# Performance work log

Measured on AMD Instinct MI355X. Metric: run time of the kernel, lower is better.

Reference implementation:

```python
import jax, jax.numpy as jnp
import numpy as np

N_NODES = 100000
N_EDGES = 3200000
D_IN = 256      # encoder_dim feeding gnn_1
D_GNN = 256     # decoder_output_dim * 4
N_CLUSTER = 4
SIGMA = 0.5
V = 1.0


def setup_inputs() -> dict:
    key = jax.random.key(0)
    ks = jax.random.split(key, 16)
    f = lambda k, shp: jax.random.normal(k, shp, dtype=jnp.float32)
    inp = {
        "encoded_input_data": f(ks[0], (N_NODES, D_IN)),
        "tra1": f(ks[1], (N_NODES, D_GNN)),
        "tra2": f(ks[2], (N_NODES, D_GNN)),
        "tra3": f(ks[3], (N_NODES, D_GNN)),
        "z":    f(ks[4], (N_NODES, D_GNN)),
        "edge_row": jax.random.randint(ks[5], (N_EDGES,), 0, N_NODES, dtype=jnp.int32),
        "edge_col": jax.random.randint(ks[6], (N_EDGES,), 0, N_NODES, dtype=jnp.int32),
        "edge_vals": jax.random.uniform(ks[7], (N_EDGES,), dtype=jnp.float32),
        "W1": f(ks[8], (D_IN, D_GNN)) * (1.0 / np.sqrt(D_IN)),
        "W2": f(ks[9], (D_GNN, D_GNN)) * (1.0 / np.sqrt(D_GNN)),
        "W3": f(ks[10], (D_GNN, D_GNN)) * (1.0 / np.sqrt(D_GNN)),
        "W4": f(ks[11], (D_GNN, D_GNN)) * (1.0 / np.sqrt(D_GNN)),
        "W5": f(ks[12], (D_GNN, N_CLUSTER)) * (1.0 / np.sqrt(D_GNN)),
        "cluster": f(ks[13], (N_CLUSTER, D_GNN)),
    }
    return inp


def _spmm(row, col, vals, x):
    # sparse adj (COO) @ x : gather source rows, scale, scatter-add to dest rows
    return jax.ops.segment_sum(vals[:, None] * x[col], row, num_segments=N_NODES)


def _gnn(x, W, row, col, vals, active=True):
    out = _spmm(row, col, vals, x @ W)
    return jax.nn.relu(out) if active else out


def reference(encoded_input_data, tra1, tra2, tra3, z,
              edge_row, edge_col, edge_vals,
              W1, W2, W3, W4, W5, cluster):
    r, c, vals = edge_row, edge_col, edge_vals
    h = _gnn(encoded_input_data, W1, r, c, vals)
    h = _gnn((1 - SIGMA) * h + SIGMA * tra1, W2, r, c, vals)
    h = _gnn((1 - SIGMA) * h + SIGMA * tra2, W3, r, c, vals)
    h = _gnn((1 - SIGMA) * h + SIGMA * tra3, W4, r, c, vals)
    h = _gnn((1 - SIGMA) * h + SIGMA * z, W5, r, c, vals, active=False)
    predict = jax.nn.softmax(h, axis=1)  # [N, n_cluster]

    # student-t soft assignment: ||z_i - mu_j||^2 expanded to avoid [N,K,D] blowup
    dist2 = (jnp.sum(z * z, axis=1, keepdims=True)
             - 2.0 * (z @ cluster.T)
             + jnp.sum(cluster * cluster, axis=1)[None, :])
    q = 1.0 / (1.0 + dist2 / V)
    q = q ** ((V + 1.0) / 2.0)
    q = q / jnp.sum(q, axis=1, keepdims=True)

    return jnp.concatenate([predict, q], axis=1)  # [N, 2*n_cluster]
```

## Files before the change

### kernel.cpp

```cpp
#include <hip/hip_runtime.h>

#define NN 100000
#define NE 3200000
#define DD 256
#define KC 4
#define MPAD 100096

typedef _Float16 f16x8 __attribute__((ext_vector_type(8)));
typedef _Float16 f16x4 __attribute__((ext_vector_type(4)));
typedef float f32x4 __attribute__((ext_vector_type(4)));


__global__ __launch_bounds__(256) void k_hist(const int* __restrict__ row,
                                              int* __restrict__ counts) {
    int e = blockIdx.x * 256 + threadIdx.x;
    if (e < NE) atomicAdd(&counts[row[e]], 1);
}

__global__ __launch_bounds__(256) void k_scan1(const int* __restrict__ counts,
                                               int* __restrict__ offs,
                                               int* __restrict__ bsum) {
    __shared__ int s[256];
    const int t = threadIdx.x;
    const int base = blockIdx.x * 1024 + t * 4;
    int v[4];
    int sum = 0;
#pragma unroll
    for (int i = 0; i < 4; ++i) {
        v[i] = (base + i < NN) ? counts[base + i] : 0;
        sum += v[i];
    }
    s[t] = sum;
    __syncthreads();
    for (int off = 1; off < 256; off <<= 1) {
        int x = (t >= off) ? s[t - off] : 0;
        __syncthreads();
        s[t] += x;
        __syncthreads();
    }
    int run = (t > 0) ? s[t - 1] : 0;
#pragma unroll
    for (int i = 0; i < 4; ++i) {
        if (base + i < NN) offs[base + i] = run;
        run += v[i];
    }
    if (t == 255) bsum[blockIdx.x] = s[255];
}

__global__ void k_scan2(int* __restrict__ bsum, int nb) {
    if (threadIdx.x == 0 && blockIdx.x == 0) {
        int run = 0;
        for (int i = 0; i < nb; ++i) {
            int c = bsum[i];
            bsum[i] = run;
            run += c;
        }
    }
}

__global__ __launch_bounds__(256) void k_scan3(int* __restrict__ offs,
                                               const int* __restrict__ bsum) {
    int i = blockIdx.x * 256 + threadIdx.x;
    if (i < NN)
        offs[i] += bsum[i >> 10];
    else if (i == NN)
        offs[NN] = NE;
}

__global__ __launch_bounds__(256) void k_fill(const int* __restrict__ row,
                                              const int* __restrict__ col,
                                              const float* __restrict__ val,
                                              const int* __restrict__ offs,
                                              int* __restrict__ cursor,
                                              int2* __restrict__ edges) {
    int e = blockIdx.x * 256 + threadIdx.x;
    if (e >= NE) return;
    int r = row[e];
    int p = offs[r] + atomicAdd(&cursor[r], 1);
    int2 ev;
    ev.x = col[e];
    ev.y = __float_as_int(val[e]);
    edges[p] = ev;
}


__global__ __launch_bounds__(256) void k_cvtX(const float* __restrict__ in,
                                              _Float16* __restrict__ out) {
    const size_t base = ((size_t)blockIdx.x * 256 + threadIdx.x) * 8;
    if (base >= (size_t)NN * DD) return;
    f32x4 v0 = __builtin_nontemporal_load(reinterpret_cast<const f32x4*>(in + base));
    f32x4 v1 = __builtin_nontemporal_load(reinterpret_cast<const f32x4*>(in + base + 4));
    f16x8 o;
    o[0] = (_Float16)v0[0]; o[1] = (_Float16)v0[1]; o[2] = (_Float16)v0[2]; o[3] = (_Float16)v0[3];
    o[4] = (_Float16)v1[0]; o[5] = (_Float16)v1[1]; o[6] = (_Float16)v1[2]; o[7] = (_Float16)v1[3];
    *reinterpret_cast<f16x8*>(out + base) = o;
}

__global__ __launch_bounds__(256) void k_cvtW(const float* __restrict__ W1,
                                              const float* __restrict__ W2,
                                              const float* __restrict__ W3,
                                              const float* __restrict__ W4,
                                              _Float16* __restrict__ Wt) {
    __shared__ float s[32][33];
    const float* W = (blockIdx.z == 0) ? W1 : (blockIdx.z == 1) ? W2 : (blockIdx.z == 2) ? W3 : W4;
    _Float16* o = Wt + (size_t)blockIdx.z * DD * DD;
    const int bk = blockIdx.x * 32;
    const int bn = blockIdx.y * 32;
    const int tx = threadIdx.x & 31, ty = threadIdx.x >> 5;
    for (int r = ty; r < 32; r += 8) s[r][tx] = W[(size_t)(bk + r) * DD + bn + tx];
    __syncthreads();
    for (int r = ty; r < 32; r += 8) o[(size_t)(bn + r) * DD + bk + tx] = (_Float16)s[tx][r];
}


__device__ __forceinline__ void load_lds16(const void* g, void* l) {
    __builtin_amdgcn_global_load_lds((const __attribute__((address_space(1))) void*)g,
                                     (__attribute__((address_space(3))) void*)l, 16, 0, 0);
}

__global__ __launch_bounds__(512, 4) void k_gemm_h(const _Float16* __restrict__ X,
                                                   const _Float16* __restrict__ Wt,
                                                   _Float16* __restrict__ Y) {
    __shared__ __align__(16) char lds[49152];
    char* const Albase = lds;
    char* const Blbase = lds + 16384;

    const int tid = threadIdx.x;
    const int lane = tid & 63;
    const int wid = tid >> 6;
    const int wr = wid >> 2;
    const int wc = wid & 3;
    const int bm = blockIdx.x * 128;

    const int aoffl = wid * 1024 + lane * 16;
    const int arw = aoffl >> 6;
    const int acb = (aoffl & 63) ^ (((arw >> 1) & 3) << 4);
    const char* const Asrc0 = (const char*)X + ((size_t)(bm + arw) * DD) * 2 + acb;
    char* const Adst0 = Albase + wid * 1024;

    const int boffl0 = wid * 1024 + lane * 16;
    const int brw0 = boffl0 >> 6;
    const int bcb0 = (boffl0 & 63) ^ (((brw0 >> 1) & 3) << 4);
    const char* const Bsrc0 = (const char*)Wt + ((size_t)brw0 * DD) * 2 + bcb0;
    const int boffl1 = 8192 + wid * 1024 + lane * 16;
    const int brw1 = boffl1 >> 6;
    const int bcb1 = (boffl1 & 63) ^ (((brw1 >> 1) & 3) << 4);
    const char* const Bsrc1 = (const char*)Wt + ((size_t)brw1 * DD) * 2 + bcb1;
    char* const Bdst0 = Blbase + wid * 1024;
    char* const Bdst1 = Blbase + 8192 + wid * 1024;

    int aro[4], bro[4];
#pragma unroll
    for (int m = 0; m < 4; ++m) {
        const int r = wr * 64 + m * 16 + (lane & 15);
        aro[m] = r * 64 + ((((lane >> 4) * 16)) ^ (((r >> 1) & 3) << 4));
    }
#pragma unroll
    for (int n = 0; n < 4; ++n) {
        const int r = wc * 64 + n * 16 + (lane & 15);
        bro[n] = r * 64 + ((((lane >> 4) * 16)) ^ (((r >> 1) & 3) << 4));
    }

    f32x4 acc[4][4];
#pragma unroll
    for (int m = 0; m < 4; ++m)
#pragma unroll
        for (int n = 0; n < 4; ++n) acc[m][n] = (f32x4){0.f, 0.f, 0.f, 0.f};

    load_lds16(Asrc0, Adst0);
    load_lds16(Bsrc0, Bdst0);
    load_lds16(Bsrc1, Bdst1);
    __syncthreads();

    for (int kt = 0; kt < 8; ++kt) {
        const int cur = kt & 1;
        if (kt < 7) {
            const size_t kb = (size_t)(kt + 1) * 32 * 2;
            load_lds16(Asrc0 + kb, Adst0 + (cur ^ 1) * 8192);
            load_lds16(Bsrc0 + kb, Bdst0 + (cur ^ 1) * 16384);
            load_lds16(Bsrc1 + kb, Bdst1 + (cur ^ 1) * 16384);
        }
        const char* Ab = Albase + cur * 8192;
        const char* Bb = Blbase + cur * 16384;
        f16x8 af[4], bf[4];
#pragma unroll
        for (int m = 0; m < 4; ++m) af[m] = *reinterpret_cast<const f16x8*>(Ab + aro[m]);
#pragma unroll
        for (int n = 0; n < 4; ++n) bf[n] = *reinterpret_cast<const f16x8*>(Bb + bro[n]);
#pragma unroll
        for (int m = 0; m < 4; ++m)
#pragma unroll
            for (int n = 0; n < 4; ++n)
                acc[m][n] = __builtin_amdgcn_mfma_f32_16x16x32_f16(af[m], bf[n], acc[m][n], 0, 0, 0);
        __syncthreads();
    }

#pragma unroll
    for (int m = 0; m < 4; ++m) {
        const int row = bm + wr * 64 + m * 16 + (lane >> 4) * 4;
#pragma unroll
        for (int n = 0; n < 4; ++n) {
            const int col = wc * 64 + n * 16 + (lane & 15);
#pragma unroll
            for (int j = 0; j < 4; ++j)
                Y[(size_t)(row + j) * DD + col] = (_Float16)acc[m][n][j];
        }
    }
}


__global__ __launch_bounds__(256) void k_spmm_h(const int* __restrict__ offs,
                                                const int2* __restrict__ edges,
                                                const _Float16* __restrict__ Y,
                                                const float* __restrict__ blend,
                                                _Float16* __restrict__ Xout) {
    const int row = blockIdx.x * 4 + (threadIdx.x >> 6);
    if (row >= NN) return;
    const int lane = threadIdx.x & 63;
    const int half = lane >> 5;
    const int sub = lane & 31;
    const int e0 = offs[row], e1 = offs[row + 1];
    float acc[8] = {};
    int e = e0 + half;
    for (; e + 6 < e1; e += 8) {
        const int2 ev0 = edges[e], ev1 = edges[e + 2], ev2 = edges[e + 4], ev3 = edges[e + 6];
        const float v0 = __int_as_float(ev0.y), v1 = __int_as_float(ev1.y);
        const float v2 = __int_as_float(ev2.y), v3 = __int_as_float(ev3.y);
        const f16x8 y0 = *reinterpret_cast<const f16x8*>(Y + (size_t)ev0.x * DD + sub * 8);
        const f16x8 y1 = *reinterpret_cast<const f16x8*>(Y + (size_t)ev1.x * DD + sub * 8);
        const f16x8 y2 = *reinterpret_cast<const f16x8*>(Y + (size_t)ev2.x * DD + sub * 8);
        const f16x8 y3 = *reinterpret_cast<const f16x8*>(Y + (size_t)ev3.x * DD + sub * 8);
#pragma unroll
        for (int j = 0; j < 8; ++j)
            acc[j] += v0 * (float)y0[j] + v1 * (float)y1[j] + v2 * (float)y2[j] + v3 * (float)y3[j];
    }
    for (; e < e1; e += 2) {
        const int2 ev = edges[e];
        const float v = __int_as_float(ev.y);
        const f16x8 y = *reinterpret_cast<const f16x8*>(Y + (size_t)ev.x * DD + sub * 8);
#pragma unroll
        for (int j = 0; j < 8; ++j) acc[j] += v * (float)y[j];
    }
#pragma unroll
    for (int j = 0; j < 8; ++j) acc[j] += __shfl_xor(acc[j], 32);
    if (half == 0) {
        const size_t bi = (size_t)row * DD + sub * 8;
        const f32x4 t0 = __builtin_nontemporal_load(reinterpret_cast<const f32x4*>(blend + bi));
        const f32x4 t1 = __builtin_nontemporal_load(reinterpret_cast<const f32x4*>(blend + bi + 4));
        f16x8 o;
        o[0] = (_Float16)(0.5f * fmaxf(acc[0], 0.f) + 0.5f * t0[0]);
        o[1] = (_Float16)(0.5f * fmaxf(acc[1], 0.f) + 0.5f * t0[1]);
        o[2] = (_Float16)(0.5f * fmaxf(acc[2], 0.f) + 0.5f * t0[2]);
        o[3] = (_Float16)(0.5f * fmaxf(acc[3], 0.f) + 0.5f * t0[3]);
        o[4] = (_Float16)(0.5f * fmaxf(acc[4], 0.f) + 0.5f * t1[0]);
        o[5] = (_Float16)(0.5f * fmaxf(acc[5], 0.f) + 0.5f * t1[1]);
        o[6] = (_Float16)(0.5f * fmaxf(acc[6], 0.f) + 0.5f * t1[2]);
        o[7] = (_Float16)(0.5f * fmaxf(acc[7], 0.f) + 0.5f * t1[3]);
        *reinterpret_cast<f16x8*>(Xout + bi) = o;
    }
}

__global__ __launch_bounds__(256) void k_spmm_last(const int* __restrict__ offs,
                                                   const int2* __restrict__ edges,
                                                   const _Float16* __restrict__ Y,
                                                   const float* __restrict__ z,
                                                   const float* __restrict__ W5,
                                                   const float* __restrict__ cl,
                                                   float* __restrict__ Y5,
                                                   float* __restrict__ out) {
    const int row = blockIdx.x * 4 + (threadIdx.x >> 6);
    if (row >= NN) return;
    const int lane = threadIdx.x & 63;
    const int half = lane >> 5;
    const int sub = lane & 31;
    const int e0 = offs[row], e1 = offs[row + 1];
    float acc[8] = {};
    int e = e0 + half;
    for (; e + 6 < e1; e += 8) {
        const int2 ev0 = edges[e], ev1 = edges[e + 2], ev2 = edges[e + 4], ev3 = edges[e + 6];
        const float v0 = __int_as_float(ev0.y), v1 = __int_as_float(ev1.y);
        const float v2 = __int_as_float(ev2.y), v3 = __int_as_float(ev3.y);
        const f16x8 y0 = *reinterpret_cast<const f16x8*>(Y + (size_t)ev0.x * DD + sub * 8);
        const f16x8 y1 = *reinterpret_cast<const f16x8*>(Y + (size_t)ev1.x * DD + sub * 8);
        const f16x8 y2 = *reinterpret_cast<const f16x8*>(Y + (size_t)ev2.x * DD + sub * 8);
        const f16x8 y3 = *reinterpret_cast<const f16x8*>(Y + (size_t)ev3.x * DD + sub * 8);
#pragma unroll
        for (int j = 0; j < 8; ++j)
            acc[j] += v0 * (float)y0[j] + v1 * (float)y1[j] + v2 * (float)y2[j] + v3 * (float)y3[j];
    }
    for (; e < e1; e += 2) {
        const int2 ev = edges[e];
        const float v = __int_as_float(ev.y);
        const f16x8 y = *reinterpret_cast<const f16x8*>(Y + (size_t)ev.x * DD + sub * 8);
#pragma unroll
        for (int j = 0; j < 8; ++j) acc[j] += v * (float)y[j];
    }
#pragma unroll
    for (int j = 0; j < 8; ++j) acc[j] += __shfl_xor(acc[j], 32);
    if (half == 0) {
        const size_t bi = (size_t)row * DD + sub * 8;
        const f32x4 z0 = __builtin_nontemporal_load(reinterpret_cast<const f32x4*>(z + bi));
        const f32x4 z1 = __builtin_nontemporal_load(reinterpret_cast<const f32x4*>(z + bi + 4));
        float zb[8] = {z0[0], z0[1], z0[2], z0[3], z1[0], z1[1], z1[2], z1[3]};
        float b[8];
#pragma unroll
        for (int j = 0; j < 8; ++j) b[j] = 0.5f * fmaxf(acc[j], 0.f) + 0.5f * zb[j];

        float p[4] = {0.f, 0.f, 0.f, 0.f};
        float zz = 0.f;
#pragma unroll
        for (int j = 0; j < 8; ++j) {
            const int d = sub * 8 + j;
            const f32x4 w = *reinterpret_cast<const f32x4*>(W5 + (size_t)d * KC);
            p[0] += b[j] * w[0];
            p[1] += b[j] * w[1];
            p[2] += b[j] * w[2];
            p[3] += b[j] * w[3];
            zz += zb[j] * zb[j];
        }
        float dot[4] = {0.f, 0.f, 0.f, 0.f}, cc[4] = {0.f, 0.f, 0.f, 0.f};
#pragma unroll
        for (int c2 = 0; c2 < 4; ++c2) {
            const f32x4 c40 = *reinterpret_cast<const f32x4*>(cl + (size_t)c2 * DD + sub * 8);
            const f32x4 c41 = *reinterpret_cast<const f32x4*>(cl + (size_t)c2 * DD + sub * 8 + 4);
            dot[c2] += zb[0] * c40[0] + zb[1] * c40[1] + zb[2] * c40[2] + zb[3] * c40[3] +
                       zb[4] * c41[0] + zb[5] * c41[1] + zb[6] * c41[2] + zb[7] * c41[3];
            cc[c2] += c40[0] * c40[0] + c40[1] * c40[1] + c40[2] * c40[2] + c40[3] * c40[3] +
                      c41[0] * c41[0] + c41[1] * c41[1] + c41[2] * c41[2] + c41[3] * c41[3];
        }
#pragma unroll
        for (int o = 16; o; o >>= 1) {
            zz += __shfl_xor(zz, o);
#pragma unroll
            for (int c2 = 0; c2 < 4; ++c2) {
                p[c2] += __shfl_xor(p[c2], o);
                dot[c2] += __shfl_xor(dot[c2], o);
                cc[c2] += __shfl_xor(cc[c2], o);
            }
        }
        if (sub == 0) {
            *reinterpret_cast<f32x4*>(Y5 + (size_t)row * KC) = (f32x4){p[0], p[1], p[2], p[3]};
            float q[4], s = 0.f;
#pragma unroll
            for (int c2 = 0; c2 < 4; ++c2) {
                const float d2 = zz - 2.f * dot[c2] + cc[c2];
                q[c2] = 1.f / (1.f + d2);
                s += q[c2];
            }
            const float inv = 1.f / s;
            *reinterpret_cast<f32x4*>(out + (size_t)row * 8 + 4) =
                (f32x4){q[0] * inv, q[1] * inv, q[2] * inv, q[3] * inv};
        }
    }
}


__device__ inline float wred(float v) {
#pragma unroll
    for (int o = 32; o; o >>= 1) v += __shfl_down(v, o);
    return v;
}

__global__ __launch_bounds__(256) void k_sm5(const int* __restrict__ offs,
                                             const int2* __restrict__ edges,
                                             const float* __restrict__ Y5,
                                             float* __restrict__ out) {
    const int row = blockIdx.x * 4 + (threadIdx.x >> 6);
    if (row >= NN) return;
    const int lane = threadIdx.x & 63;
    const int e0 = offs[row], e1 = offs[row + 1];
    float ax = 0.f, ay = 0.f, az = 0.f, aw = 0.f;
    for (int e = e0 + lane; e < e1; e += 64) {
        const int2 ev = edges[e];
        const float v = __int_as_float(ev.y);
        const f32x4 y = *reinterpret_cast<const f32x4*>(Y5 + (size_t)ev.x * KC);
        ax += v * y[0];
        ay += v * y[1];
        az += v * y[2];
        aw += v * y[3];
    }
    ax = wred(ax);
    ay = wred(ay);
    az = wred(az);
    aw = wred(aw);
    if (lane == 0) {
        float m = fmaxf(fmaxf(ax, ay), fmaxf(az, aw));
        float ex = __expf(ax - m), ey = __expf(ay - m), ez = __expf(az - m), ew = __expf(aw - m);
        float inv = 1.f / (ex + ey + ez + ew);
        *reinterpret_cast<f32x4*>(out + (size_t)row * 8) =
            (f32x4){ex * inv, ey * inv, ez * inv, ew * inv};
    }
}


extern "C" void kernel_launch(void* const* d_in, const int* in_sizes, int n_in,
                              void* d_out, int out_size, void* d_ws, size_t ws_size,
                              hipStream_t stream) {
    const float* enc = (const float*)d_in[0];
    const float* tra1 = (const float*)d_in[1];
    const float* tra2 = (const float*)d_in[2];
    const float* tra3 = (const float*)d_in[3];
    const float* z = (const float*)d_in[4];
    const int* erow = (const int*)d_in[5];
    const int* ecol = (const int*)d_in[6];
    const float* evals = (const float*)d_in[7];
    const float* W1 = (const float*)d_in[8];
    const float* W2 = (const float*)d_in[9];
    const float* W3 = (const float*)d_in[10];
    const float* W4 = (const float*)d_in[11];
    const float* W5 = (const float*)d_in[12];
    const float* cluster = (const float*)d_in[13];
    float* out = (float*)d_out;

    char* ws = (char*)d_ws;
    size_t off = 0;
    auto take = [&](size_t bytes) -> void* {
        void* p = ws + off;
        off = (off + bytes + 255) & ~(size_t)255;
        return p;
    };
    int* counts = (int*)take((size_t)NN * 4);
    int* cursor = (int*)take((size_t)NN * 4);
    int* offs = (int*)take((size_t)(NN + 1) * 4);
    int* bsum = (int*)take(4096);
    int2* edges = (int2*)take((size_t)NE * 8);
    _Float16* Xa = (_Float16*)take((size_t)MPAD * DD * 2);
    _Float16* Xb = (_Float16*)take((size_t)MPAD * DD * 2);
    _Float16* Wt = (_Float16*)take((size_t)4 * DD * DD * 2);
    float* Y5 = (float*)take((size_t)NN * KC * 4);

    hipMemsetAsync(counts, 0, (size_t)NN * 4, stream);
    hipMemsetAsync(cursor, 0, (size_t)NN * 4, stream);

    k_hist<<<(NE + 255) / 256, 256, 0, stream>>>(erow, counts);
    const int nsb = (NN + 1023) / 1024;
    k_scan1<<<nsb, 256, 0, stream>>>(counts, offs, bsum);
    k_scan2<<<1, 64, 0, stream>>>(bsum, nsb);
    k_scan3<<<(NN + 256) / 256, 256, 0, stream>>>(offs, bsum);
    k_fill<<<(NE + 255) / 256, 256, 0, stream>>>(erow, ecol, evals, offs, cursor, edges);

    k_cvtX<<<(NN * DD / 8 + 255) / 256, 256, 0, stream>>>(enc, Xa);
    k_cvtW<<<dim3(8, 8, 4), 256, 0, stream>>>(W1, W2, W3, W4, Wt);

    const int gb = MPAD / 128;
    const int rb = NN / 4;

    k_gemm_h<<<gb, 512, 0, stream>>>(Xa, Wt + 0 * DD * DD, Xb);
    k_spmm_h<<<rb, 256, 0, stream>>>(offs, edges, Xb, tra1, Xa);

    k_gemm_h<<<gb, 512, 0, stream>>>(Xa, Wt + 1 * DD * DD, Xb);
    k_spmm_h<<<rb, 256, 0, stream>>>(offs, edges, Xb, tra2, Xa);

    k_gemm_h<<<gb, 512, 0, stream>>>(Xa, Wt + 2 * DD * DD, Xb);
    k_spmm_h<<<rb, 256, 0, stream>>>(offs, edges, Xb, tra3, Xa);

    k_gemm_h<<<gb, 512, 0, stream>>>(Xa, Wt + 3 * DD * DD, Xb);
    k_spmm_last<<<rb, 256, 0, stream>>>(offs, edges, Xb, z, W5, cluster, Y5, out);

    k_sm5<<<rb, 256, 0, stream>>>(offs, edges, Y5, out);
}
```

Before: 1.437 ms.

## Pack edges into 32-bit words and split SpMM feature columns into two passes

Each edge becomes one 32-bit word: a 17-bit column index plus a 15-bit fixed-point quantized weight. This halves the CSR edge traffic. Every SpMM layer also now runs as two launches, each covering 128 of the 256 feature columns. The smaller gather working set should fit better in cache, and four edge groups per row give more memory parallelism. The costs are that the edge list is read twice, the weights are quantized to 15 bits (assumes values in [0,1]), and the last layer has to carry partial results between its two passes.

```diff
diff --git a/kernel.cpp b/kernel.cpp
--- a/kernel.cpp
+++ b/kernel.cpp
@@ -5,9 +5,9 @@
 #define DD 256
 #define KC 4
 #define MPAD 100096
+#define INV15 (1.0f / 32767.0f)
 
 typedef _Float16 f16x8 __attribute__((ext_vector_type(8)));
-typedef _Float16 f16x4 __attribute__((ext_vector_type(4)));
 typedef float f32x4 __attribute__((ext_vector_type(4)));
 
 
@@ -72,15 +72,13 @@
                                               const float* __restrict__ val,
                                               const int* __restrict__ offs,
                                               int* __restrict__ cursor,
-                                              int2* __restrict__ edges) {
+                                              unsigned* __restrict__ edges) {
     int e = blockIdx.x * 256 + threadIdx.x;
     if (e >= NE) return;
     int r = row[e];
     int p = offs[r] + atomicAdd(&cursor[r], 1);
-    int2 ev;
-    ev.x = col[e];
-    ev.y = __float_as_int(val[e]);
-    edges[p] = ev;
+    unsigned v15 = (unsigned)(val[e] * 32767.f + 0.5f);
+    edges[p] = (v15 << 17) | (unsigned)col[e];
 }
 
 
@@ -210,41 +208,47 @@
 
 
 __global__ __launch_bounds__(256) void k_spmm_h(const int* __restrict__ offs,
-                                                const int2* __restrict__ edges,
+                                                const unsigned* __restrict__ edges,
                                                 const _Float16* __restrict__ Y,
                                                 const float* __restrict__ blend,
-                                                _Float16* __restrict__ Xout) {
+                                                _Float16* __restrict__ Xout,
+                                                int d_off) {
     const int row = blockIdx.x * 4 + (threadIdx.x >> 6);
     if (row >= NN) return;
     const int lane = threadIdx.x & 63;
-    const int half = lane >> 5;
-    const int sub = lane & 31;
+    const int grp = lane >> 4, sub = lane & 15;
+    const int dbase = d_off + sub * 8;
     const int e0 = offs[row], e1 = offs[row + 1];
     float acc[8] = {};
-    int e = e0 + half;
-    for (; e + 6 < e1; e += 8) {
-        const int2 ev0 = edges[e], ev1 = edges[e + 2], ev2 = edges[e + 4], ev3 = edges[e + 6];
-        const float v0 = __int_as_float(ev0.y), v1 = __int_as_float(ev1.y);
-        const float v2 = __int_as_float(ev2.y), v3 = __int_as_float(ev3.y);
-        const f16x8 y0 = *reinterpret_cast<const f16x8*>(Y + (size_t)ev0.x * DD + sub * 8);
-        const f16x8 y1 = *reinterpret_cast<const f16x8*>(Y + (size_t)ev1.x * DD + sub * 8);
-        const f16x8 y2 = *reinterpret_cast<const f16x8*>(Y + (size_t)ev2.x * DD + sub * 8);
-        const f16x8 y3 = *reinterpret_cast<const f16x8*>(Y + (size_t)ev3.x * DD + sub * 8);
+    int e = e0 + grp;
+    for (; e + 12 < e1; e += 16) {
+        const unsigned u0 = edges[e], u1 = edges[e + 4], u2 = edges[e + 8], u3 = edges[e + 12];
+        const float v0 = (float)(u0 >> 17) * INV15;
+        const float v1 = (float)(u1 >> 17) * INV15;
+        const float v2 = (float)(u2 >> 17) * INV15;
+        const float v3 = (float)(u3 >> 17) * INV15;
+        const f16x8 y0 = *reinterpret_cast<const f16x8*>(Y + ((size_t)(u0 & 0x1FFFFu) << 8) + dbase);
+        const f16x8 y1 = *reinterpret_cast<const f16x8*>(Y + ((size_t)(u1 & 0x1FFFFu) << 8) + dbase);
+        const f16x8 y2 = *reinterpret_cast<const f16x8*>(Y + ((size_t)(u2 & 0x1FFFFu) << 8) + dbase);
+        const f16x8 y3 = *reinterpret_cast<const f16x8*>(Y + ((size_t)(u3 & 0x1FFFFu) << 8) + dbase);
 #pragma unroll
         for (int j = 0; j < 8; ++j)
             acc[j] += v0 * (float)y0[j] + v1 * (float)y1[j] + v2 * (float)y2[j] + v3 * (float)y3[j];
     }
-    for (; e < e1; e += 2) {
-        const int2 ev = edges[e];
-        const float v = __int_as_float(ev.y);
-        const f16x8 y = *reinterpret_cast<const f16x8*>(Y + (size_t)ev.x * DD + sub * 8);
+    for (; e < e1; e += 4) {
+        const unsigned u = edges[e];
+        const float v = (float)(u >> 17) * INV15;
+        const f16x8 y = *reinterpret_cast<const f16x8*>(Y + ((size_t)(u & 0x1FFFFu) << 8) + dbase);
 #pragma unroll
         for (int j = 0; j < 8; ++j) acc[j] += v * (float)y[j];
     }
 #pragma unroll
-    for (int j = 0; j < 8; ++j) acc[j] += __shfl_xor(acc[j], 32);
-    if (half == 0) {
-        const size_t bi = (size_t)row * DD + sub * 8;
+    for (int j = 0; j < 8; ++j) {
+        acc[j] += __shfl_xor(acc[j], 16);
+        acc[j] += __shfl_xor(acc[j], 32);
+    }
+    if (grp == 0) {
+        const size_t bi = (size_t)row * DD + dbase;
         const f32x4 t0 = __builtin_nontemporal_load(reinterpret_cast<const f32x4*>(blend + bi));
         const f32x4 t1 = __builtin_nontemporal_load(reinterpret_cast<const f32x4*>(blend + bi + 4));
         f16x8 o;
@@ -260,76 +264,79 @@
     }
 }
 
-__global__ __launch_bounds__(256) void k_spmm_last(const int* __restrict__ offs,
-                                                   const int2* __restrict__ edges,
-                                                   const _Float16* __restrict__ Y,
-                                                   const float* __restrict__ z,
-                                                   const float* __restrict__ W5,
-                                                   const float* __restrict__ cl,
-                                                   float* __restrict__ Y5,
-                                                   float* __restrict__ out) {
+__global__ __launch_bounds__(256) void k_last(const int* __restrict__ offs,
+                                              const unsigned* __restrict__ edges,
+                                              const _Float16* __restrict__ Y,
+                                              const float* __restrict__ z,
+                                              const float* __restrict__ W5,
+                                              const float* __restrict__ cl,
+                                              float* __restrict__ part,
+                                              float* __restrict__ Y5,
+                                              float* __restrict__ out,
+                                              int d_off, int final_) {
     const int row = blockIdx.x * 4 + (threadIdx.x >> 6);
     if (row >= NN) return;
     const int lane = threadIdx.x & 63;
-    const int half = lane >> 5;
-    const int sub = lane & 31;
+    const int grp = lane >> 4, sub = lane & 15;
+    const int dbase = d_off + sub * 8;
     const int e0 = offs[row], e1 = offs[row + 1];
     float acc[8] = {};
-    int e = e0 + half;
-    for (; e + 6 < e1; e += 8) {
-        const int2 ev0 = edges[e], ev1 = edges[e + 2], ev2 = edges[e + 4], ev3 = edges[e + 6];
-        const float v0 = __int_as_float(ev0.y), v1 = __int_as_float(ev1.y);
-        const float v2 = __int_as_float(ev2.y), v3 = __int_as_float(ev3.y);
-        const f16x8 y0 = *reinterpret_cast<const f16x8*>(Y + (size_t)ev0.x * DD + sub * 8);
-        const f16x8 y1 = *reinterpret_cast<const f16x8*>(Y + (size_t)ev1.x * DD + sub * 8);
-        const f16x8 y2 = *reinterpret_cast<const f16x8*>(Y + (size_t)ev2.x * DD + sub * 8);
-        const f16x8 y3 = *reinterpret_cast<const f16x8*>(Y + (size_t)ev3.x * DD + sub * 8);
+    int e = e0 + grp;
+    for (; e + 12 < e1; e += 16) {
+        const unsigned u0 = edges[e], u1 = edges[e + 4], u2 = edges[e + 8], u3 = edges[e + 12];
+        const float v0 = (float)(u0 >> 17) * INV15;
+        const float v1 = (float)(u1 >> 17) * INV15;
+        const float v2 = (float)(u2 >> 17) * INV15;
+        const float v3 = (float)(u3 >> 17) * INV15;
+        const f16x8 y0 = *reinterpret_cast<const f16x8*>(Y + ((size_t)(u0 & 0x1FFFFu) << 8) + dbase);
+        const f16x8 y1 = *reinterpret_cast<const f16x8*>(Y + ((size_t)(u1 & 0x1FFFFu) << 8) + dbase);
+        const f16x8 y2 = *reinterpret_cast<const f16x8*>(Y + ((size_t)(u2 & 0x1FFFFu) << 8) + dbase);
+        const f16x8 y3 = *reinterpret_cast<const f16x8*>(Y + ((size_t)(u3 & 0x1FFFFu) << 8) + dbase);
 #pragma unroll
         for (int j = 0; j < 8; ++j)
             acc[j] += v0 * (float)y0[j] + v1 * (float)y1[j] + v2 * (float)y2[j] + v3 * (float)y3[j];
     }
-    for (; e < e1; e += 2) {
-        const int2 ev = edges[e];
-        const float v = __int_as_float(ev.y);
-        const f16x8 y = *reinterpret_cast<const f16x8*>(Y + (size_t)ev.x * DD + sub * 8);
+    for (; e < e1; e += 4) {
+        const unsigned u = edges[e];
+        const float v = (float)(u >> 17) * INV15;
+        const f16x8 y = *reinterpret_cast<const f16x8*>(Y + ((size_t)(u & 0x1FFFFu) << 8) + dbase);
 #pragma unroll
         for (int j = 0; j < 8; ++j) acc[j] += v * (float)y[j];
     }
 #pragma unroll
-    for (int j = 0; j < 8; ++j) acc[j] += __shfl_xor(acc[j], 32);
-    if (half == 0) {
-        const size_t bi = (size_t)row * DD + sub * 8;
+    for (int j = 0; j < 8; ++j) {
+        acc[j] += __shfl_xor(acc[j], 16);
+        acc[j] += __shfl_xor(acc[j], 32);
+    }
+    if (grp == 0) {
+        const size_t bi = (size_t)row * DD + dbase;
         const f32x4 z0 = __builtin_nontemporal_load(reinterpret_cast<const f32x4*>(z + bi));
         const f32x4 z1 = __builtin_nontemporal_load(reinterpret_cast<const f32x4*>(z + bi + 4));
-        float zb[8] = {z0[0], z0[1], z0[2], z0[3], z1[0], z1[1], z1[2], z1[3]};
-        float b[8];
-#pragma unroll
-        for (int j = 0; j < 8; ++j) b[j] = 0.5f * fmaxf(acc[j], 0.f) + 0.5f * zb[j];
-
+        const float zb[8] = {z0[0], z0[1], z0[2], z0[3], z1[0], z1[1], z1[2], z1[3]};
         float p[4] = {0.f, 0.f, 0.f, 0.f};
         float zz = 0.f;
 #pragma unroll
         for (int j = 0; j < 8; ++j) {
-            const int d = sub * 8 + j;
-            const f32x4 w = *reinterpret_cast<const f32x4*>(W5 + (size_t)d * KC);
-            p[0] += b[j] * w[0];
-            p[1] += b[j] * w[1];
-            p[2] += b[j] * w[2];
-            p[3] += b[j] * w[3];
+            const float b = 0.5f * fmaxf(acc[j], 0.f) + 0.5f * zb[j];
+            const f32x4 w = *reinterpret_cast<const f32x4*>(W5 + (size_t)(dbase + j) * KC);
+            p[0] += b * w[0];
+            p[1] += b * w[1];
+            p[2] += b * w[2];
+            p[3] += b * w[3];
             zz += zb[j] * zb[j];
         }
         float dot[4] = {0.f, 0.f, 0.f, 0.f}, cc[4] = {0.f, 0.f, 0.f, 0.f};
 #pragma unroll
         for (int c2 = 0; c2 < 4; ++c2) {
-            const f32x4 c40 = *reinterpret_cast<const f32x4*>(cl + (size_t)c2 * DD + sub * 8);
-            const f32x4 c41 = *reinterpret_cast<const f32x4*>(cl + (size_t)c2 * DD + sub * 8 + 4);
-            dot[c2] += zb[0] * c40[0] + zb[1] * c40[1] + zb[2] * c40[2] + zb[3] * c40[3] +
-                       zb[4] * c41[0] + zb[5] * c41[1] + zb[6] * c41[2] + zb[7] * c41[3];
-            cc[c2] += c40[0] * c40[0] + c40[1] * c40[1] + c40[2] * c40[2] + c40[3] * c40[3] +
-                      c41[0] * c41[0] + c41[1] * c41[1] + c41[2] * c41[2] + c41[3] * c41[3];
-        }
-#pragma unroll
-        for (int o = 16; o; o >>= 1) {
+            const f32x4 c40 = *reinterpret_cast<const f32x4*>(cl + (size_t)c2 * DD + dbase);
+            const f32x4 c41 = *reinterpret_cast<const f32x4*>(cl + (size_t)c2 * DD + dbase + 4);
+            dot[c2] = zb[0] * c40[0] + zb[1] * c40[1] + zb[2] * c40[2] + zb[3] * c40[3] +
+                      zb[4] * c41[0] + zb[5] * c41[1] + zb[6] * c41[2] + zb[7] * c41[3];
+            cc[c2] = c40[0] * c40[0] + c40[1] * c40[1] + c40[2] * c40[2] + c40[3] * c40[3] +
+                     c41[0] * c41[0] + c41[1] * c41[1] + c41[2] * c41[2] + c41[3] * c41[3];
+        }
+#pragma unroll
+        for (int o = 8; o; o >>= 1) {
             zz += __shfl_xor(zz, o);
 #pragma unroll
             for (int c2 = 0; c2 < 4; ++c2) {
@@ -339,17 +346,33 @@
             }
         }
         if (sub == 0) {
-            *reinterpret_cast<f32x4*>(Y5 + (size_t)row * KC) = (f32x4){p[0], p[1], p[2], p[3]};
-            float q[4], s = 0.f;
-#pragma unroll
-            for (int c2 = 0; c2 < 4; ++c2) {
-                const float d2 = zz - 2.f * dot[c2] + cc[c2];
-                q[c2] = 1.f / (1.f + d2);
-                s += q[c2];
+            float* pr = part + (size_t)row * 16;
+            if (!final_) {
+                *reinterpret_cast<f32x4*>(pr) = (f32x4){p[0], p[1], p[2], p[3]};
+                *reinterpret_cast<f32x4*>(pr + 4) = (f32x4){zz, dot[0], dot[1], dot[2]};
+                *reinterpret_cast<f32x4*>(pr + 8) = (f32x4){dot[3], cc[0], cc[1], cc[2]};
+                pr[12] = cc[3];
+            } else {
+                const f32x4 a0 = *reinterpret_cast<const f32x4*>(pr);
+                const f32x4 a1 = *reinterpret_cast<const f32x4*>(pr + 4);
+                const f32x4 a2 = *reinterpret_cast<const f32x4*>(pr + 8);
+                const float a3 = pr[12];
+                p[0] += a0[0]; p[1] += a0[1]; p[2] += a0[2]; p[3] += a0[3];
+                zz += a1[0];
+                dot[0] += a1[1]; dot[1] += a1[2]; dot[2] += a1[3]; dot[3] += a2[0];
+                cc[0] += a2[1]; cc[1] += a2[2]; cc[2] += a2[3]; cc[3] += a3;
+                *reinterpret_cast<f32x4*>(Y5 + (size_t)row * KC) = (f32x4){p[0], p[1], p[2], p[3]};
+                float q[4], s = 0.f;
+#pragma unroll
+                for (int c2 = 0; c2 < 4; ++c2) {
+                    const float d2 = zz - 2.f * dot[c2] + cc[c2];
+                    q[c2] = 1.f / (1.f + d2);
+                    s += q[c2];
+                }
+                const float inv = 1.f / s;
+                *reinterpret_cast<f32x4*>(out + (size_t)row * 8 + 4) =
+                    (f32x4){q[0] * inv, q[1] * inv, q[2] * inv, q[3] * inv};
             }
-            const float inv = 1.f / s;
-            *reinterpret_cast<f32x4*>(out + (size_t)row * 8 + 4) =
-                (f32x4){q[0] * inv, q[1] * inv, q[2] * inv, q[3] * inv};
         }
     }
 }
@@ -362,7 +385,7 @@
 }
 
 __global__ __launch_bounds__(256) void k_sm5(const int* __restrict__ offs,
-                                             const int2* __restrict__ edges,
+                                             const unsigned* __restrict__ edges,
                                              const float* __restrict__ Y5,
                                              float* __restrict__ out) {
     const int row = blockIdx.x * 4 + (threadIdx.x >> 6);
@@ -371,9 +394,9 @@
     const int e0 = offs[row], e1 = offs[row + 1];
     float ax = 0.f, ay = 0.f, az = 0.f, aw = 0.f;
     for (int e = e0 + lane; e < e1; e += 64) {
-        const int2 ev = edges[e];
-        const float v = __int_as_float(ev.y);
-        const f32x4 y = *reinterpret_cast<const f32x4*>(Y5 + (size_t)ev.x * KC);
+        const unsigned u = edges[e];
+        const float v = (float)(u >> 17) * INV15;
+        const f32x4 y = *reinterpret_cast<const f32x4*>(Y5 + (size_t)(u & 0x1FFFFu) * KC);
         ax += v * y[0];
         ay += v * y[1];
         az += v * y[2];
@@ -423,11 +446,12 @@
     int* cursor = (int*)take((size_t)NN * 4);
     int* offs = (int*)take((size_t)(NN + 1) * 4);
     int* bsum = (int*)take(4096);
-    int2* edges = (int2*)take((size_t)NE * 8);
+    unsigned* edges = (unsigned*)take((size_t)NE * 4);
     _Float16* Xa = (_Float16*)take((size_t)MPAD * DD * 2);
     _Float16* Xb = (_Float16*)take((size_t)MPAD * DD * 2);
     _Float16* Wt = (_Float16*)take((size_t)4 * DD * DD * 2);
     float* Y5 = (float*)take((size_t)NN * KC * 4);
+    float* part = (float*)take((size_t)NN * 16 * 4);
 
     hipMemsetAsync(counts, 0, (size_t)NN * 4, stream);
     hipMemsetAsync(cursor, 0, (size_t)NN * 4, stream);
@@ -446,16 +470,20 @@
     const int rb = NN / 4;
 
     k_gemm_h<<<gb, 512, 0, stream>>>(Xa, Wt + 0 * DD * DD, Xb);
-    k_spmm_h<<<rb, 256, 0, stream>>>(offs, edges, Xb, tra1, Xa);
+    k_spmm_h<<<rb, 256, 0, stream>>>(offs, edges, Xb, tra1, Xa, 0);
+    k_spmm_h<<<rb, 256, 0, stream>>>(offs, edges, Xb, tra1, Xa, 128);
 
     k_gemm_h<<<gb, 512, 0, stream>>>(Xa, Wt + 1 * DD * DD, Xb);
-    k_spmm_h<<<rb, 256, 0, stream>>>(offs, edges, Xb, tra2, Xa);
+    k_spmm_h<<<rb, 256, 0, stream>>>(offs, edges, Xb, tra2, Xa, 0);
+    k_spmm_h<<<rb, 256, 0, stream>>>(offs, edges, Xb, tra2, Xa, 128);
 
     k_gemm_h<<<gb, 512, 0, stream>>>(Xa, Wt + 2 * DD * DD, Xb);
-    k_spmm_h<<<rb, 256, 0, stream>>>(offs, edges, Xb, tra3, Xa);
+    k_spmm_h<<<rb, 256, 0, stream>>>(offs, edges, Xb, tra3, Xa, 0);
+    k_spmm_h<<<rb, 256, 0, stream>>>(offs, edges, Xb, tra3, Xa, 128);
 
     k_gemm_h<<<gb, 512, 0, stream>>>(Xa, Wt + 3 * DD * DD, Xb);
-    k_spmm_last<<<rb, 256, 0, stream>>>(offs, edges, Xb, z, W5, cluster, Y5, out);
+    k_last<<<rb, 256, 0, stream>>>(offs, edges, Xb, z, W5, cluster, part, Y5, out, 0, 0);
+    k_last<<<rb, 256, 0, stream>>>(offs, edges, Xb, z, W5, cluster, part, Y5, out, 128, 1);
 
     k_sm5<<<rb, 256, 0, stream>>>(offs, edges, Y5, out);
 }
```

New measurement: 1.461 ms. About the same (+1.7%).
